# Kernel tuning notes

Measured on AMD Instinct MI355X. Metric: run time of the kernel, lower is better.

Reference implementation:

```python
import jax, jax.numpy as jnp
import numpy as np

N_NODES = 50000
N_EDGES = 800000
IN_DIM = 96
HID = 96
OUT_DIM = 32
N_GRAPHS = 256


def setup_inputs() -> dict:
    key = jax.random.key(0)
    ks = jax.random.split(key, 12)
    x = jax.random.normal(ks[0], (N_NODES, IN_DIM), dtype=jnp.float32)
    edge_index = jax.random.randint(ks[1], (2, N_EDGES), 0, N_NODES, dtype=jnp.int64)
    batch = jnp.sort(jax.random.randint(ks[2], (N_NODES,), 0, N_GRAPHS, dtype=jnp.int64))
    s = 1.0 / np.sqrt(HID)
    W1 = jax.random.normal(ks[3], (IN_DIM, HID), dtype=jnp.float32) * s
    W2 = jax.random.normal(ks[4], (HID, HID), dtype=jnp.float32) * s
    W3 = jax.random.normal(ks[5], (HID, HID), dtype=jnp.float32) * s
    fc_w = jax.random.normal(ks[6], (HID, OUT_DIM), dtype=jnp.float32) * s
    return {
        'x': x, 'edge_index': edge_index, 'batch': batch,
        'W1': W1, 'b1': jnp.zeros((HID,), jnp.float32),
        'W2': W2, 'b2': jnp.zeros((HID,), jnp.float32),
        'W3': W3, 'b3': jnp.zeros((HID,), jnp.float32),
        'fc_w': fc_w, 'fc_b': jnp.zeros((OUT_DIM,), jnp.float32),
    }


def _gcn_conv(h, row, col, norm, W, b, n_nodes):
    # linear transform first (PyG GCNConv), then normalized gather/scatter-add
    h = h @ W                                   # [N, F]
    msg = h[row] * norm[:, None]                # [E+N, F] gather + scale
    out = jax.ops.segment_sum(msg, col, num_segments=n_nodes)
    return out + b


def reference(x, edge_index, batch, W1, b1, W2, b2, W3, b3, fc_w, fc_b):
    n = x.shape[0]
    loop = jnp.arange(n, dtype=edge_index.dtype)
    row = jnp.concatenate([edge_index[0], loop])  # sources (with self-loops)
    col = jnp.concatenate([edge_index[1], loop])  # targets
    # symmetric normalization: deg over targets, norm = d^-1/2[row] * d^-1/2[col]
    deg = jax.ops.segment_sum(jnp.ones_like(col, dtype=x.dtype), col, num_segments=n)
    dis = jnp.where(deg > 0, jax.lax.rsqrt(deg), 0.0)
    norm = dis[row] * dis[col]

    h = jax.nn.relu(_gcn_conv(x, row, col, norm, W1, b1, n))
    h = jax.nn.relu(_gcn_conv(h, row, col, norm, W2, b2, n))
    h = jax.nn.relu(_gcn_conv(h, row, col, norm, W3, b3, n))

    # global_mean_pool over graph ids
    sums = jax.ops.segment_sum(h, batch, num_segments=N_GRAPHS)
    cnts = jax.ops.segment_sum(jnp.ones((n,), h.dtype), batch, num_segments=N_GRAPHS)
    pooled = sums / jnp.maximum(cnts, 1.0)[:, None]
    return pooled @ fc_w + fc_b
```

## Files before the change

kernel.cpp:

```cpp
#include <hip/hip_runtime.h>

#define NN 50000
#define NE 800000
#define F  96
#define F4 24
#define FB 48
#define RB4 12
#define OD 32
#define NG 256
#define CAP 64
#define PROWS 21
#define SHARDS 8
#define SHARD_SZ 6250
#define PERSHARD 64
#define GL 12
#define NWF 1152

typedef unsigned int u32;
typedef unsigned short u16;
typedef short short8 __attribute__((ext_vector_type(8)));
typedef float f32x4 __attribute__((ext_vector_type(4)));

static inline size_t align_up(size_t x) { return (x + 255) & ~(size_t)255; }

__device__ inline u32 f2bf_rne(float x) {
    u32 u = __float_as_uint(x);
    return (u + 0x7fffu + ((u >> 16) & 1u)) >> 16;
}
__device__ inline u32 packbf(float a, float b) {
    return f2bf_rne(a) | (f2bf_rne(b) << 16);
}
__device__ inline float bf_lo(u32 u) { return __uint_as_float(u << 16); }
__device__ inline float bf_hi(u32 u) { return __uint_as_float(u & 0xffff0000u); }

__global__ __launch_bounds__(256) void k_fillb(const int* __restrict__ src,
                                               const int* __restrict__ tgt,
                                               int* __restrict__ cnt,
                                               u16* __restrict__ bucket) {
    int shard = blockIdx.x & (SHARDS - 1);
    int sb    = blockIdx.x >> 3;
    int lo    = shard * SHARD_SZ;
    int hi    = lo + SHARD_SZ;
    const int4* tgt4 = reinterpret_cast<const int4*>(tgt);
    const int4* src4 = reinterpret_cast<const int4*>(src);
    const int nchunk = NE / 4;
    for (int c = sb * 256 + threadIdx.x; c < nchunk; c += PERSHARD * 256) {
        int4 t4 = tgt4[c];
        int4 s4 = src4[c];
        if (t4.x >= lo && t4.x < hi) {
            int p = atomicAdd(&cnt[t4.x], 1);
            if (p < CAP) bucket[t4.x * CAP + p] = (u16)s4.x;
        }
        if (t4.y >= lo && t4.y < hi) {
            int p = atomicAdd(&cnt[t4.y], 1);
            if (p < CAP) bucket[t4.y * CAP + p] = (u16)s4.y;
        }
        if (t4.z >= lo && t4.z < hi) {
            int p = atomicAdd(&cnt[t4.z], 1);
            if (p < CAP) bucket[t4.z * CAP + p] = (u16)s4.z;
        }
        if (t4.w >= lo && t4.w < hi) {
            int p = atomicAdd(&cnt[t4.w], 1);
            if (p < CAP) bucket[t4.w * CAP + p] = (u16)s4.w;
        }
    }
}

__global__ __launch_bounds__(256) void k_dis(const int* __restrict__ cnt, float* __restrict__ dis) {
    int i = blockIdx.x * 256 + threadIdx.x;
    if (i < NN) dis[i] = rsqrtf((float)(cnt[i] + 1));
}

__global__ __launch_bounds__(256) void k_cvt(const float4* __restrict__ x4,
                                             uint4* __restrict__ xb4) {
    int i = blockIdx.x * 256 + threadIdx.x;
    if (i >= NN * RB4) return;
    float4 f0 = x4[(size_t)i * 2];
    float4 f1 = x4[(size_t)i * 2 + 1];
    xb4[i] = make_uint4(packbf(f0.x, f0.y), packbf(f0.z, f0.w),
                        packbf(f1.x, f1.y), packbf(f1.z, f1.w));
}

__global__ __launch_bounds__(256) void k_wprep(const float* __restrict__ W,
                                               uint4* __restrict__ wfragG) {
    int e = blockIdx.x * 256 + threadIdx.x;
    if (e >= NWF) return;
    int n  = e & 15;
    int t1 = e >> 4;
    int quad = t1 & 3;
    int t2 = t1 >> 2;
    int kc = t2 % 3;
    int ct = t2 / 3;
    int k  = kc * 32 + quad * 8;
    int col = ct * 16 + n;
    u32 w0 = packbf(W[(k + 0) * F + col], W[(k + 1) * F + col]);
    u32 w1 = packbf(W[(k + 2) * F + col], W[(k + 3) * F + col]);
    u32 w2 = packbf(W[(k + 4) * F + col], W[(k + 5) * F + col]);
    u32 w3 = packbf(W[(k + 6) * F + col], W[(k + 7) * F + col]);
    wfragG[e] = make_uint4(w0, w1, w2, w3);
}

__global__ __launch_bounds__(256) void k_gemm_mfma(const uint4* __restrict__ Ab4,
                                                   const uint4* __restrict__ wfragG,
                                                   const float* __restrict__ dis,
                                                   u16* __restrict__ Cb16) {
    __shared__ uint4 wfrag[NWF];
    __shared__ uint4 atile[64 * 13];
    int tid = threadIdx.x;
    int r0 = blockIdx.x * 64;
    for (int i = tid; i < NWF; i += 256) wfrag[i] = wfragG[i];
    for (int i = tid; i < 64 * RB4; i += 256) {
        int r = i / RB4, j = i - r * RB4;
        int row = r0 + r;
        atile[r * 13 + j] = (row < NN) ? Ab4[(size_t)row * RB4 + j]
                                       : make_uint4(0u, 0u, 0u, 0u);
    }
    __syncthreads();

    int wave = tid >> 6;
    int lane = tid & 63;
    int m    = lane & 15;
    int quad = lane >> 4;
    int arow = wave * 16 + m;

    short8 a0 = *reinterpret_cast<const short8*>(&atile[arow * 13 + 0 * 4 + quad]);
    short8 a1 = *reinterpret_cast<const short8*>(&atile[arow * 13 + 1 * 4 + quad]);
    short8 a2 = *reinterpret_cast<const short8*>(&atile[arow * 13 + 2 * 4 + quad]);

    f32x4 acc[6];
#pragma unroll
    for (int ct = 0; ct < 6; ++ct) acc[ct] = (f32x4)(0.0f);

#pragma unroll
    for (int ct = 0; ct < 6; ++ct) {
        short8 b0 = *reinterpret_cast<const short8*>(&wfrag[((ct * 3 + 0) * 4 + quad) * 16 + m]);
        short8 b1 = *reinterpret_cast<const short8*>(&wfrag[((ct * 3 + 1) * 4 + quad) * 16 + m]);
        short8 b2 = *reinterpret_cast<const short8*>(&wfrag[((ct * 3 + 2) * 4 + quad) * 16 + m]);
        acc[ct] = __builtin_amdgcn_mfma_f32_16x16x32_bf16(a0, b0, acc[ct], 0, 0, 0);
        acc[ct] = __builtin_amdgcn_mfma_f32_16x16x32_bf16(a1, b1, acc[ct], 0, 0, 0);
        acc[ct] = __builtin_amdgcn_mfma_f32_16x16x32_bf16(a2, b2, acc[ct], 0, 0, 0);
    }

    int rbase = r0 + wave * 16 + quad * 4;
    float dr[4];
#pragma unroll
    for (int r = 0; r < 4; ++r) dr[r] = (rbase + r < NN) ? dis[rbase + r] : 0.0f;
#pragma unroll
    for (int ct = 0; ct < 6; ++ct) {
#pragma unroll
        for (int r = 0; r < 4; ++r) {
            int row = rbase + r;
            if (row < NN)
                Cb16[(size_t)row * F + ct * 16 + m] = (u16)f2bf_rne(acc[ct][r] * dr[r]);
        }
    }
}

__global__ __launch_bounds__(256) void k_gather(const u32* __restrict__ hb,
                                                const int* __restrict__ cnt,
                                                const u16* __restrict__ bucket,
                                                const float* __restrict__ dis,
                                                const float* __restrict__ bias,
                                                uint4* __restrict__ outb4) {
    int idx = blockIdx.x * 256 + threadIdx.x;
    if (idx >= NN * GL) return;
    int v   = idx / GL;
    int sub = idx - v * GL;
    int co  = sub * 4;

    uint4 hv = *reinterpret_cast<const uint4*>(&hb[(size_t)v * FB + co]);
    float a0 = bf_lo(hv.x), a1 = bf_hi(hv.x);
    float a2 = bf_lo(hv.y), a3 = bf_hi(hv.y);
    float a4 = bf_lo(hv.z), a5 = bf_hi(hv.z);
    float a6 = bf_lo(hv.w), a7 = bf_hi(hv.w);

    int deg = cnt[v];
    if (deg > CAP) deg = CAP;
    const u16* bkt = &bucket[v * CAP];

    int e = 0;
    for (; e + 7 < deg; e += 8) {
        uint4 b8 = *reinterpret_cast<const uint4*>(&bkt[e]);
        int s0 = b8.x & 0xffff, s1 = b8.x >> 16;
        int s2 = b8.y & 0xffff, s3 = b8.y >> 16;
        int s4 = b8.z & 0xffff, s5 = b8.z >> 16;
        int s6 = b8.w & 0xffff, s7 = b8.w >> 16;
        uint4 g0 = *reinterpret_cast<const uint4*>(&hb[(size_t)s0 * FB + co]);
        uint4 g1 = *reinterpret_cast<const uint4*>(&hb[(size_t)s1 * FB + co]);
        uint4 g2 = *reinterpret_cast<const uint4*>(&hb[(size_t)s2 * FB + co]);
        uint4 g3 = *reinterpret_cast<const uint4*>(&hb[(size_t)s3 * FB + co]);
        uint4 g4 = *reinterpret_cast<const uint4*>(&hb[(size_t)s4 * FB + co]);
        uint4 g5 = *reinterpret_cast<const uint4*>(&hb[(size_t)s5 * FB + co]);
        uint4 g6 = *reinterpret_cast<const uint4*>(&hb[(size_t)s6 * FB + co]);
        uint4 g7 = *reinterpret_cast<const uint4*>(&hb[(size_t)s7 * FB + co]);
        a0 += bf_lo(g0.x) + bf_lo(g1.x) + bf_lo(g2.x) + bf_lo(g3.x)
            + bf_lo(g4.x) + bf_lo(g5.x) + bf_lo(g6.x) + bf_lo(g7.x);
        a1 += bf_hi(g0.x) + bf_hi(g1.x) + bf_hi(g2.x) + bf_hi(g3.x)
            + bf_hi(g4.x) + bf_hi(g5.x) + bf_hi(g6.x) + bf_hi(g7.x);
        a2 += bf_lo(g0.y) + bf_lo(g1.y) + bf_lo(g2.y) + bf_lo(g3.y)
            + bf_lo(g4.y) + bf_lo(g5.y) + bf_lo(g6.y) + bf_lo(g7.y);
        a3 += bf_hi(g0.y) + bf_hi(g1.y) + bf_hi(g2.y) + bf_hi(g3.y)
            + bf_hi(g4.y) + bf_hi(g5.y) + bf_hi(g6.y) + bf_hi(g7.y);
        a4 += bf_lo(g0.z) + bf_lo(g1.z) + bf_lo(g2.z) + bf_lo(g3.z)
            + bf_lo(g4.z) + bf_lo(g5.z) + bf_lo(g6.z) + bf_lo(g7.z);
        a5 += bf_hi(g0.z) + bf_hi(g1.z) + bf_hi(g2.z) + bf_hi(g3.z)
            + bf_hi(g4.z) + bf_hi(g5.z) + bf_hi(g6.z) + bf_hi(g7.z);
        a6 += bf_lo(g0.w) + bf_lo(g1.w) + bf_lo(g2.w) + bf_lo(g3.w)
            + bf_lo(g4.w) + bf_lo(g5.w) + bf_lo(g6.w) + bf_lo(g7.w);
        a7 += bf_hi(g0.w) + bf_hi(g1.w) + bf_hi(g2.w) + bf_hi(g3.w)
            + bf_hi(g4.w) + bf_hi(g5.w) + bf_hi(g6.w) + bf_hi(g7.w);
    }
    for (; e + 3 < deg; e += 4) {
        uint2 b4 = *reinterpret_cast<const uint2*>(&bkt[e]);
        int s0 = b4.x & 0xffff, s1 = b4.x >> 16;
        int s2 = b4.y & 0xffff, s3 = b4.y >> 16;
        uint4 g0 = *reinterpret_cast<const uint4*>(&hb[(size_t)s0 * FB + co]);
        uint4 g1 = *reinterpret_cast<const uint4*>(&hb[(size_t)s1 * FB + co]);
        uint4 g2 = *reinterpret_cast<const uint4*>(&hb[(size_t)s2 * FB + co]);
        uint4 g3 = *reinterpret_cast<const uint4*>(&hb[(size_t)s3 * FB + co]);
        a0 += bf_lo(g0.x) + bf_lo(g1.x) + bf_lo(g2.x) + bf_lo(g3.x);
        a1 += bf_hi(g0.x) + bf_hi(g1.x) + bf_hi(g2.x) + bf_hi(g3.x);
        a2 += bf_lo(g0.y) + bf_lo(g1.y) + bf_lo(g2.y) + bf_lo(g3.y);
        a3 += bf_hi(g0.y) + bf_hi(g1.y) + bf_hi(g2.y) + bf_hi(g3.y);
        a4 += bf_lo(g0.z) + bf_lo(g1.z) + bf_lo(g2.z) + bf_lo(g3.z);
        a5 += bf_hi(g0.z) + bf_hi(g1.z) + bf_hi(g2.z) + bf_hi(g3.z);
        a6 += bf_lo(g0.w) + bf_lo(g1.w) + bf_lo(g2.w) + bf_lo(g3.w);
        a7 += bf_hi(g0.w) + bf_hi(g1.w) + bf_hi(g2.w) + bf_hi(g3.w);
    }
    for (; e < deg; ++e) {
        int s = bkt[e];
        uint4 g = *reinterpret_cast<const uint4*>(&hb[(size_t)s * FB + co]);
        a0 += bf_lo(g.x); a1 += bf_hi(g.x);
        a2 += bf_lo(g.y); a3 += bf_hi(g.y);
        a4 += bf_lo(g.z); a5 += bf_hi(g.z);
        a6 += bf_lo(g.w); a7 += bf_hi(g.w);
    }
    float dv = dis[v];
    const float4* bb = reinterpret_cast<const float4*>(bias);
    float4 b0 = bb[sub * 2], b1 = bb[sub * 2 + 1];
    float o0 = fmaxf(dv * a0 + b0.x, 0.0f);
    float o1 = fmaxf(dv * a1 + b0.y, 0.0f);
    float o2 = fmaxf(dv * a2 + b0.z, 0.0f);
    float o3 = fmaxf(dv * a3 + b0.w, 0.0f);
    float o4 = fmaxf(dv * a4 + b1.x, 0.0f);
    float o5 = fmaxf(dv * a5 + b1.y, 0.0f);
    float o6 = fmaxf(dv * a6 + b1.z, 0.0f);
    float o7 = fmaxf(dv * a7 + b1.w, 0.0f);
    outb4[(size_t)v * RB4 + sub] = make_uint4(packbf(o0, o1), packbf(o2, o3),
                                              packbf(o4, o5), packbf(o6, o7));
}

__device__ inline int lower_bound_i(const int* __restrict__ a, int n, int key) {
    int lo = 0, hi = n;
    while (lo < hi) {
        int mid = (lo + hi) >> 1;
        if (a[mid] < key) lo = mid + 1; else hi = mid;
    }
    return lo;
}

__global__ __launch_bounds__(512) void k_pool(const uint2* __restrict__ hb2,
                                              const int* __restrict__ batch,
                                              float4* __restrict__ pooled4) {
    __shared__ int range[2];
    __shared__ float4 part[PROWS][F4];
    int g = blockIdx.x;
    int t = threadIdx.x;
    if (t == 0) range[0] = lower_bound_i(batch, NN, g);
    if (t == 1) range[1] = lower_bound_i(batch, NN, g + 1);
    __syncthreads();
    int lo = range[0], hi = range[1];
    int row = t / F4;
    int sub = t - row * F4;
    if (row < PROWS) {
        float4 acc = make_float4(0.f, 0.f, 0.f, 0.f);
        for (int v = lo + row; v < hi; v += PROWS) {
            uint2 xv = hb2[(size_t)v * F4 + sub];
            acc.x += bf_lo(xv.x); acc.y += bf_hi(xv.x);
            acc.z += bf_lo(xv.y); acc.w += bf_hi(xv.y);
        }
        part[row][sub] = acc;
    }
    __syncthreads();
    if (t < F4) {
        float4 s = part[0][t];
        for (int r = 1; r < PROWS; ++r) {
            float4 p = part[r][t];
            s.x += p.x; s.y += p.y; s.z += p.z; s.w += p.w;
        }
        float inv = 1.0f / fmaxf((float)(hi - lo), 1.0f);
        s.x *= inv; s.y *= inv; s.z *= inv; s.w *= inv;
        pooled4[g * F4 + t] = s;
    }
}

__global__ __launch_bounds__(256) void k_fc(const float* __restrict__ pooled,
                                            const float* __restrict__ fcw,
                                            const float* __restrict__ fcb,
                                            float* __restrict__ out) {
    int i = blockIdx.x * 256 + threadIdx.x;
    if (i >= NG * OD) return;
    int g = i >> 5;
    int o = i & 31;
    float acc = 0.0f;
    for (int f = 0; f < F; ++f) acc += pooled[g * F + f] * fcw[f * OD + o];
    out[i] = acc + fcb[o];
}

extern "C" void kernel_launch(void* const* d_in, const int* in_sizes, int n_in,
                              void* d_out, int out_size, void* d_ws, size_t ws_size,
                              hipStream_t stream) {
    (void)in_sizes; (void)n_in; (void)out_size; (void)ws_size;
    const float* x    = (const float*)d_in[0];
    const int*   ei   = (const int*)d_in[1];
    const int*   batc = (const int*)d_in[2];
    const float* W1   = (const float*)d_in[3];
    const float* b1   = (const float*)d_in[4];
    const float* W2   = (const float*)d_in[5];
    const float* b2   = (const float*)d_in[6];
    const float* W3   = (const float*)d_in[7];
    const float* b3   = (const float*)d_in[8];
    const float* fcw  = (const float*)d_in[9];
    const float* fcb  = (const float*)d_in[10];
    float* out = (float*)d_out;

    const int* src = ei;
    const int* tgt = ei + NE;

    char* ws = (char*)d_ws;
    int*    cnt    = (int*)ws;    ws += align_up((size_t)NN * 4);
    float*  dis    = (float*)ws;  ws += align_up((size_t)NN * 4);
    u16*    bucket = (u16*)ws;    ws += align_up((size_t)NN * CAP * 2);
    u32*    hlinb  = (u32*)ws;    ws += align_up((size_t)NN * FB * 4);
    u32*    xb     = (u32*)ws;    ws += align_up((size_t)NN * FB * 4);
    uint4*  wfragG = (uint4*)ws;  ws += align_up((size_t)NWF * 16);
    float*  pooled = (float*)ws;  ws += align_up((size_t)NG * F * 4);

    const int B = 256;
    const int node_grid = (NN + B - 1) / B;
    const int gemm_grid = (NN + 63) / 64;
    const int gath_grid = (NN * GL + B - 1) / B;
    const int cvt_grid  = (NN * RB4 + B - 1) / B;
    const int wprep_grid = (NWF + B - 1) / B;

    (void)hipMemsetAsync(cnt, 0, (size_t)NN * 4, stream);
    k_fillb<<<SHARDS * PERSHARD, B, 0, stream>>>(src, tgt, cnt, bucket);
    k_dis  <<<node_grid, B, 0, stream>>>(cnt, dis);
    k_cvt  <<<cvt_grid, B, 0, stream>>>((const float4*)x, (uint4*)xb);

    k_wprep<<<wprep_grid, B, 0, stream>>>(W1, wfragG);
    k_gemm_mfma<<<gemm_grid, B, 0, stream>>>((const uint4*)xb, wfragG, dis, (u16*)hlinb);
    k_gather<<<gath_grid, B, 0, stream>>>(hlinb, cnt, bucket, dis, b1, (uint4*)xb);

    k_wprep<<<wprep_grid, B, 0, stream>>>(W2, wfragG);
    k_gemm_mfma<<<gemm_grid, B, 0, stream>>>((const uint4*)xb, wfragG, dis, (u16*)hlinb);
    k_gather<<<gath_grid, B, 0, stream>>>(hlinb, cnt, bucket, dis, b2, (uint4*)xb);

    k_wprep<<<wprep_grid, B, 0, stream>>>(W3, wfragG);
    k_gemm_mfma<<<gemm_grid, B, 0, stream>>>((const uint4*)xb, wfragG, dis, (u16*)hlinb);
    k_gather<<<gath_grid, B, 0, stream>>>(hlinb, cnt, bucket, dis, b3, (uint4*)xb);

    k_pool<<<NG, 512, 0, stream>>>((const uint2*)xb, batc, (float4*)pooled);
    k_fc  <<<(NG * OD + B - 1) / B, B, 0, stream>>>(pooled, fcw, fcb, out);
}
```

Baseline: 263.8 us.

## Fuse aggregation and GEMM per layer using aggregate-then-transform ordering

Reorders each GCN layer to aggregate the dis-prescaled features first and then multiply by W, so one kernel does the gather into shared memory followed by the MFMA GEMM with bias, ReLU and next-layer dis scaling in the epilogue. The separate gemm and gather kernels and the intermediate hlin buffer round trip are removed, and the three weight preps are merged into one launch. The cost is a per-block 18KB weight fragment load into LDS for only 32 rows, and the gather's latency is no longer overlapped across separate launches. Rounding also changes slightly because features are stored in bf16 after pre-scaling.

```diff
diff --git a/kernel.cpp b/kernel.cpp
--- a/kernel.cpp
+++ b/kernel.cpp
@@ -13,8 +13,9 @@
 #define SHARDS 8
 #define SHARD_SZ 6250
 #define PERSHARD 64
-#define GL 12
 #define NWF 1152
+#define RPB 32
+#define TPB 128
 
 typedef unsigned int u32;
 typedef unsigned short u16;
@@ -72,21 +73,29 @@
 }
 
 __global__ __launch_bounds__(256) void k_cvt(const float4* __restrict__ x4,
-                                             uint4* __restrict__ xb4) {
+                                             const float* __restrict__ dis,
+                                             uint4* __restrict__ rb4) {
     int i = blockIdx.x * 256 + threadIdx.x;
     if (i >= NN * RB4) return;
+    int v = i / RB4;
+    float dv = dis[v];
     float4 f0 = x4[(size_t)i * 2];
     float4 f1 = x4[(size_t)i * 2 + 1];
-    xb4[i] = make_uint4(packbf(f0.x, f0.y), packbf(f0.z, f0.w),
-                        packbf(f1.x, f1.y), packbf(f1.z, f1.w));
-}
-
-__global__ __launch_bounds__(256) void k_wprep(const float* __restrict__ W,
-                                               uint4* __restrict__ wfragG) {
+    rb4[i] = make_uint4(packbf(dv * f0.x, dv * f0.y), packbf(dv * f0.z, dv * f0.w),
+                        packbf(dv * f1.x, dv * f1.y), packbf(dv * f1.z, dv * f1.w));
+}
+
+__global__ __launch_bounds__(256) void k_wprep3(const float* __restrict__ W1,
+                                                const float* __restrict__ W2,
+                                                const float* __restrict__ W3,
+                                                uint4* __restrict__ wf) {
     int e = blockIdx.x * 256 + threadIdx.x;
-    if (e >= NWF) return;
-    int n  = e & 15;
-    int t1 = e >> 4;
+    if (e >= 3 * NWF) return;
+    int wi = e / NWF;
+    int f  = e - wi * NWF;
+    const float* W = (wi == 0) ? W1 : ((wi == 1) ? W2 : W3);
+    int n  = f & 15;
+    int t1 = f >> 4;
     int quad = t1 & 3;
     int t2 = t1 >> 2;
     int kc = t2 % 3;
@@ -97,23 +106,105 @@
     u32 w1 = packbf(W[(k + 2) * F + col], W[(k + 3) * F + col]);
     u32 w2 = packbf(W[(k + 4) * F + col], W[(k + 5) * F + col]);
     u32 w3 = packbf(W[(k + 6) * F + col], W[(k + 7) * F + col]);
-    wfragG[e] = make_uint4(w0, w1, w2, w3);
-}
-
-__global__ __launch_bounds__(256) void k_gemm_mfma(const uint4* __restrict__ Ab4,
-                                                   const uint4* __restrict__ wfragG,
-                                                   const float* __restrict__ dis,
-                                                   u16* __restrict__ Cb16) {
+    wf[e] = make_uint4(w0, w1, w2, w3);
+}
+
+__global__ __launch_bounds__(TPB) void k_layer(const uint4* __restrict__ rprev,
+                                               const uint4* __restrict__ wfragG,
+                                               const int* __restrict__ cnt,
+                                               const u16* __restrict__ bucket,
+                                               const float* __restrict__ dis,
+                                               const float* __restrict__ bias,
+                                               const int last,
+                                               u16* __restrict__ rnext) {
     __shared__ uint4 wfrag[NWF];
-    __shared__ uint4 atile[64 * 13];
+    __shared__ uint4 atile[RPB * 13];
     int tid = threadIdx.x;
-    int r0 = blockIdx.x * 64;
-    for (int i = tid; i < NWF; i += 256) wfrag[i] = wfragG[i];
-    for (int i = tid; i < 64 * RB4; i += 256) {
-        int r = i / RB4, j = i - r * RB4;
-        int row = r0 + r;
-        atile[r * 13 + j] = (row < NN) ? Ab4[(size_t)row * RB4 + j]
-                                       : make_uint4(0u, 0u, 0u, 0u);
+    int r0 = blockIdx.x * RPB;
+    for (int i = tid; i < NWF; i += TPB) wfrag[i] = wfragG[i];
+
+    const u32* hb = reinterpret_cast<const u32*>(rprev);
+
+#pragma unroll
+    for (int it = 0; it < 3; ++it) {
+        int slot = it * TPB + tid;
+        int ln  = slot / 12;
+        int sub = slot - ln * 12;
+        int v = r0 + ln;
+        uint4 res = make_uint4(0u, 0u, 0u, 0u);
+        if (v < NN) {
+            int co = sub * 4;
+            uint4 hv = *reinterpret_cast<const uint4*>(&hb[(size_t)v * FB + co]);
+            float a0 = bf_lo(hv.x), a1 = bf_hi(hv.x);
+            float a2 = bf_lo(hv.y), a3 = bf_hi(hv.y);
+            float a4 = bf_lo(hv.z), a5 = bf_hi(hv.z);
+            float a6 = bf_lo(hv.w), a7 = bf_hi(hv.w);
+
+            int deg = cnt[v];
+            if (deg > CAP) deg = CAP;
+            const u16* bkt = &bucket[v * CAP];
+            int e = 0;
+            for (; e + 7 < deg; e += 8) {
+                uint4 b8 = *reinterpret_cast<const uint4*>(&bkt[e]);
+                int s0 = b8.x & 0xffff, s1 = b8.x >> 16;
+                int s2 = b8.y & 0xffff, s3 = b8.y >> 16;
+                int s4 = b8.z & 0xffff, s5 = b8.z >> 16;
+                int s6 = b8.w & 0xffff, s7 = b8.w >> 16;
+                uint4 g0 = *reinterpret_cast<const uint4*>(&hb[(size_t)s0 * FB + co]);
+                uint4 g1 = *reinterpret_cast<const uint4*>(&hb[(size_t)s1 * FB + co]);
+                uint4 g2 = *reinterpret_cast<const uint4*>(&hb[(size_t)s2 * FB + co]);
+                uint4 g3 = *reinterpret_cast<const uint4*>(&hb[(size_t)s3 * FB + co]);
+                uint4 g4 = *reinterpret_cast<const uint4*>(&hb[(size_t)s4 * FB + co]);
+                uint4 g5 = *reinterpret_cast<const uint4*>(&hb[(size_t)s5 * FB + co]);
+                uint4 g6 = *reinterpret_cast<const uint4*>(&hb[(size_t)s6 * FB + co]);
+                uint4 g7 = *reinterpret_cast<const uint4*>(&hb[(size_t)s7 * FB + co]);
+                a0 += bf_lo(g0.x) + bf_lo(g1.x) + bf_lo(g2.x) + bf_lo(g3.x)
+                    + bf_lo(g4.x) + bf_lo(g5.x) + bf_lo(g6.x) + bf_lo(g7.x);
+                a1 += bf_hi(g0.x) + bf_hi(g1.x) + bf_hi(g2.x) + bf_hi(g3.x)
+                    + bf_hi(g4.x) + bf_hi(g5.x) + bf_hi(g6.x) + bf_hi(g7.x);
+                a2 += bf_lo(g0.y) + bf_lo(g1.y) + bf_lo(g2.y) + bf_lo(g3.y)
+                    + bf_lo(g4.y) + bf_lo(g5.y) + bf_lo(g6.y) + bf_lo(g7.y);
+                a3 += bf_hi(g0.y) + bf_hi(g1.y) + bf_hi(g2.y) + bf_hi(g3.y)
+                    + bf_hi(g4.y) + bf_hi(g5.y) + bf_hi(g6.y) + bf_hi(g7.y);
+                a4 += bf_lo(g0.z) + bf_lo(g1.z) + bf_lo(g2.z) + bf_lo(g3.z)
+                    + bf_lo(g4.z) + bf_lo(g5.z) + bf_lo(g6.z) + bf_lo(g7.z);
+                a5 += bf_hi(g0.z) + bf_hi(g1.z) + bf_hi(g2.z) + bf_hi(g3.z)
+                    + bf_hi(g4.z) + bf_hi(g5.z) + bf_hi(g6.z) + bf_hi(g7.z);
+                a6 += bf_lo(g0.w) + bf_lo(g1.w) + bf_lo(g2.w) + bf_lo(g3.w)
+                    + bf_lo(g4.w) + bf_lo(g5.w) + bf_lo(g6.w) + bf_lo(g7.w);
+                a7 += bf_hi(g0.w) + bf_hi(g1.w) + bf_hi(g2.w) + bf_hi(g3.w)
+                    + bf_hi(g4.w) + bf_hi(g5.w) + bf_hi(g6.w) + bf_hi(g7.w);
+            }
+            for (; e + 3 < deg; e += 4) {
+                uint2 b4 = *reinterpret_cast<const uint2*>(&bkt[e]);
+                int s0 = b4.x & 0xffff, s1 = b4.x >> 16;
+                int s2 = b4.y & 0xffff, s3 = b4.y >> 16;
+                uint4 g0 = *reinterpret_cast<const uint4*>(&hb[(size_t)s0 * FB + co]);
+                uint4 g1 = *reinterpret_cast<const uint4*>(&hb[(size_t)s1 * FB + co]);
+                uint4 g2 = *reinterpret_cast<const uint4*>(&hb[(size_t)s2 * FB + co]);
+                uint4 g3 = *reinterpret_cast<const uint4*>(&hb[(size_t)s3 * FB + co]);
+                a0 += bf_lo(g0.x) + bf_lo(g1.x) + bf_lo(g2.x) + bf_lo(g3.x);
+                a1 += bf_hi(g0.x) + bf_hi(g1.x) + bf_hi(g2.x) + bf_hi(g3.x);
+                a2 += bf_lo(g0.y) + bf_lo(g1.y) + bf_lo(g2.y) + bf_lo(g3.y);
+                a3 += bf_hi(g0.y) + bf_hi(g1.y) + bf_hi(g2.y) + bf_hi(g3.y);
+                a4 += bf_lo(g0.z) + bf_lo(g1.z) + bf_lo(g2.z) + bf_lo(g3.z);
+                a5 += bf_hi(g0.z) + bf_hi(g1.z) + bf_hi(g2.z) + bf_hi(g3.z);
+                a6 += bf_lo(g0.w) + bf_lo(g1.w) + bf_lo(g2.w) + bf_lo(g3.w);
+                a7 += bf_hi(g0.w) + bf_hi(g1.w) + bf_hi(g2.w) + bf_hi(g3.w);
+            }
+            for (; e < deg; ++e) {
+                int s = bkt[e];
+                uint4 g = *reinterpret_cast<const uint4*>(&hb[(size_t)s * FB + co]);
+                a0 += bf_lo(g.x); a1 += bf_hi(g.x);
+                a2 += bf_lo(g.y); a3 += bf_hi(g.y);
+                a4 += bf_lo(g.z); a5 += bf_hi(g.z);
+                a6 += bf_lo(g.w); a7 += bf_hi(g.w);
+            }
+            float dv = dis[v];
+            res = make_uint4(packbf(dv * a0, dv * a1), packbf(dv * a2, dv * a3),
+                             packbf(dv * a4, dv * a5), packbf(dv * a6, dv * a7));
+        }
+        atile[ln * 13 + sub] = res;
     }
     __syncthreads();
 
@@ -130,7 +221,6 @@
     f32x4 acc[6];
 #pragma unroll
     for (int ct = 0; ct < 6; ++ct) acc[ct] = (f32x4)(0.0f);
-
 #pragma unroll
     for (int ct = 0; ct < 6; ++ct) {
         short8 b0 = *reinterpret_cast<const short8*>(&wfrag[((ct * 3 + 0) * 4 + quad) * 16 + m]);
@@ -144,110 +234,22 @@
     int rbase = r0 + wave * 16 + quad * 4;
     float dr[4];
 #pragma unroll
-    for (int r = 0; r < 4; ++r) dr[r] = (rbase + r < NN) ? dis[rbase + r] : 0.0f;
+    for (int r = 0; r < 4; ++r) {
+        int row = rbase + r;
+        dr[r] = (row < NN) ? (last ? 1.0f : dis[row]) : 0.0f;
+    }
 #pragma unroll
     for (int ct = 0; ct < 6; ++ct) {
+        float bb = bias[ct * 16 + m];
 #pragma unroll
         for (int r = 0; r < 4; ++r) {
             int row = rbase + r;
-            if (row < NN)
-                Cb16[(size_t)row * F + ct * 16 + m] = (u16)f2bf_rne(acc[ct][r] * dr[r]);
-        }
-    }
-}
-
-__global__ __launch_bounds__(256) void k_gather(const u32* __restrict__ hb,
-                                                const int* __restrict__ cnt,
-                                                const u16* __restrict__ bucket,
-                                                const float* __restrict__ dis,
-                                                const float* __restrict__ bias,
-                                                uint4* __restrict__ outb4) {
-    int idx = blockIdx.x * 256 + threadIdx.x;
-    if (idx >= NN * GL) return;
-    int v   = idx / GL;
-    int sub = idx - v * GL;
-    int co  = sub * 4;
-
-    uint4 hv = *reinterpret_cast<const uint4*>(&hb[(size_t)v * FB + co]);
-    float a0 = bf_lo(hv.x), a1 = bf_hi(hv.x);
-    float a2 = bf_lo(hv.y), a3 = bf_hi(hv.y);
-    float a4 = bf_lo(hv.z), a5 = bf_hi(hv.z);
-    float a6 = bf_lo(hv.w), a7 = bf_hi(hv.w);
-
-    int deg = cnt[v];
-    if (deg > CAP) deg = CAP;
-    const u16* bkt = &bucket[v * CAP];
-
-    int e = 0;
-    for (; e + 7 < deg; e += 8) {
-        uint4 b8 = *reinterpret_cast<const uint4*>(&bkt[e]);
-        int s0 = b8.x & 0xffff, s1 = b8.x >> 16;
-        int s2 = b8.y & 0xffff, s3 = b8.y >> 16;
-        int s4 = b8.z & 0xffff, s5 = b8.z >> 16;
-        int s6 = b8.w & 0xffff, s7 = b8.w >> 16;
-        uint4 g0 = *reinterpret_cast<const uint4*>(&hb[(size_t)s0 * FB + co]);
-        uint4 g1 = *reinterpret_cast<const uint4*>(&hb[(size_t)s1 * FB + co]);
-        uint4 g2 = *reinterpret_cast<const uint4*>(&hb[(size_t)s2 * FB + co]);
-        uint4 g3 = *reinterpret_cast<const uint4*>(&hb[(size_t)s3 * FB + co]);
-        uint4 g4 = *reinterpret_cast<const uint4*>(&hb[(size_t)s4 * FB + co]);
-        uint4 g5 = *reinterpret_cast<const uint4*>(&hb[(size_t)s5 * FB + co]);
-        uint4 g6 = *reinterpret_cast<const uint4*>(&hb[(size_t)s6 * FB + co]);
-        uint4 g7 = *reinterpret_cast<const uint4*>(&hb[(size_t)s7 * FB + co]);
-        a0 += bf_lo(g0.x) + bf_lo(g1.x) + bf_lo(g2.x) + bf_lo(g3.x)
-            + bf_lo(g4.x) + bf_lo(g5.x) + bf_lo(g6.x) + bf_lo(g7.x);
-        a1 += bf_hi(g0.x) + bf_hi(g1.x) + bf_hi(g2.x) + bf_hi(g3.x)
-            + bf_hi(g4.x) + bf_hi(g5.x) + bf_hi(g6.x) + bf_hi(g7.x);
-        a2 += bf_lo(g0.y) + bf_lo(g1.y) + bf_lo(g2.y) + bf_lo(g3.y)
-            + bf_lo(g4.y) + bf_lo(g5.y) + bf_lo(g6.y) + bf_lo(g7.y);
-        a3 += bf_hi(g0.y) + bf_hi(g1.y) + bf_hi(g2.y) + bf_hi(g3.y)
-            + bf_hi(g4.y) + bf_hi(g5.y) + bf_hi(g6.y) + bf_hi(g7.y);
-        a4 += bf_lo(g0.z) + bf_lo(g1.z) + bf_lo(g2.z) + bf_lo(g3.z)
-            + bf_lo(g4.z) + bf_lo(g5.z) + bf_lo(g6.z) + bf_lo(g7.z);
-        a5 += bf_hi(g0.z) + bf_hi(g1.z) + bf_hi(g2.z) + bf_hi(g3.z)
-            + bf_hi(g4.z) + bf_hi(g5.z) + bf_hi(g6.z) + bf_hi(g7.z);
-        a6 += bf_lo(g0.w) + bf_lo(g1.w) + bf_lo(g2.w) + bf_lo(g3.w)
-            + bf_lo(g4.w) + bf_lo(g5.w) + bf_lo(g6.w) + bf_lo(g7.w);
-        a7 += bf_hi(g0.w) + bf_hi(g1.w) + bf_hi(g2.w) + bf_hi(g3.w)
-            + bf_hi(g4.w) + bf_hi(g5.w) + bf_hi(g6.w) + bf_hi(g7.w);
-    }
-    for (; e + 3 < deg; e += 4) {
-        uint2 b4 = *reinterpret_cast<const uint2*>(&bkt[e]);
-        int s0 = b4.x & 0xffff, s1 = b4.x >> 16;
-        int s2 = b4.y & 0xffff, s3 = b4.y >> 16;
-        uint4 g0 = *reinterpret_cast<const uint4*>(&hb[(size_t)s0 * FB + co]);
-        uint4 g1 = *reinterpret_cast<const uint4*>(&hb[(size_t)s1 * FB + co]);
-        uint4 g2 = *reinterpret_cast<const uint4*>(&hb[(size_t)s2 * FB + co]);
-        uint4 g3 = *reinterpret_cast<const uint4*>(&hb[(size_t)s3 * FB + co]);
-        a0 += bf_lo(g0.x) + bf_lo(g1.x) + bf_lo(g2.x) + bf_lo(g3.x);
-        a1 += bf_hi(g0.x) + bf_hi(g1.x) + bf_hi(g2.x) + bf_hi(g3.x);
-        a2 += bf_lo(g0.y) + bf_lo(g1.y) + bf_lo(g2.y) + bf_lo(g3.y);
-        a3 += bf_hi(g0.y) + bf_hi(g1.y) + bf_hi(g2.y) + bf_hi(g3.y);
-        a4 += bf_lo(g0.z) + bf_lo(g1.z) + bf_lo(g2.z) + bf_lo(g3.z);
-        a5 += bf_hi(g0.z) + bf_hi(g1.z) + bf_hi(g2.z) + bf_hi(g3.z);
-        a6 += bf_lo(g0.w) + bf_lo(g1.w) + bf_lo(g2.w) + bf_lo(g3.w);
-        a7 += bf_hi(g0.w) + bf_hi(g1.w) + bf_hi(g2.w) + bf_hi(g3.w);
-    }
-    for (; e < deg; ++e) {
-        int s = bkt[e];
-        uint4 g = *reinterpret_cast<const uint4*>(&hb[(size_t)s * FB + co]);
-        a0 += bf_lo(g.x); a1 += bf_hi(g.x);
-        a2 += bf_lo(g.y); a3 += bf_hi(g.y);
-        a4 += bf_lo(g.z); a5 += bf_hi(g.z);
-        a6 += bf_lo(g.w); a7 += bf_hi(g.w);
-    }
-    float dv = dis[v];
-    const float4* bb = reinterpret_cast<const float4*>(bias);
-    float4 b0 = bb[sub * 2], b1 = bb[sub * 2 + 1];
-    float o0 = fmaxf(dv * a0 + b0.x, 0.0f);
-    float o1 = fmaxf(dv * a1 + b0.y, 0.0f);
-    float o2 = fmaxf(dv * a2 + b0.z, 0.0f);
-    float o3 = fmaxf(dv * a3 + b0.w, 0.0f);
-    float o4 = fmaxf(dv * a4 + b1.x, 0.0f);
-    float o5 = fmaxf(dv * a5 + b1.y, 0.0f);
-    float o6 = fmaxf(dv * a6 + b1.z, 0.0f);
-    float o7 = fmaxf(dv * a7 + b1.w, 0.0f);
-    outb4[(size_t)v * RB4 + sub] = make_uint4(packbf(o0, o1), packbf(o2, o3),
-                                              packbf(o4, o5), packbf(o6, o7));
+            if (row < NN) {
+                float h = fmaxf(acc[ct][r] + bb, 0.0f);
+                rnext[(size_t)row * F + ct * 16 + m] = (u16)f2bf_rne(h * dr[r]);
+            }
+        }
+    }
 }
 
 __device__ inline int lower_bound_i(const int* __restrict__ a, int n, int key) {
@@ -331,35 +333,30 @@
     int*    cnt    = (int*)ws;    ws += align_up((size_t)NN * 4);
     float*  dis    = (float*)ws;  ws += align_up((size_t)NN * 4);
     u16*    bucket = (u16*)ws;    ws += align_up((size_t)NN * CAP * 2);
-    u32*    hlinb  = (u32*)ws;    ws += align_up((size_t)NN * FB * 4);
-    u32*    xb     = (u32*)ws;    ws += align_up((size_t)NN * FB * 4);
-    uint4*  wfragG = (uint4*)ws;  ws += align_up((size_t)NWF * 16);
+    u32*    rA     = (u32*)ws;    ws += align_up((size_t)NN * FB * 4);
+    u32*    rB     = (u32*)ws;    ws += align_up((size_t)NN * FB * 4);
+    uint4*  wfrag3 = (uint4*)ws;  ws += align_up((size_t)3 * NWF * 16);
     float*  pooled = (float*)ws;  ws += align_up((size_t)NG * F * 4);
 
     const int B = 256;
-    const int node_grid = (NN + B - 1) / B;
-    const int gemm_grid = (NN + 63) / 64;
-    const int gath_grid = (NN * GL + B - 1) / B;
-    const int cvt_grid  = (NN * RB4 + B - 1) / B;
-    const int wprep_grid = (NWF + B - 1) / B;
+    const int node_grid  = (NN + B - 1) / B;
+    const int cvt_grid   = (NN * RB4 + B - 1) / B;
+    const int wprep_grid = (3 * NWF + B - 1) / B;
+    const int layer_grid = (NN + RPB - 1) / RPB;
 
     (void)hipMemsetAsync(cnt, 0, (size_t)NN * 4, stream);
-    k_fillb<<<SHARDS * PERSHARD, B, 0, stream>>>(src, tgt, cnt, bucket);
-    k_dis  <<<node_grid, B, 0, stream>>>(cnt, dis);
-    k_cvt  <<<cvt_grid, B, 0, stream>>>((const float4*)x, (uint4*)xb);
-
-    k_wprep<<<wprep_grid, B, 0, stream>>>(W1, wfragG);
-    k_gemm_mfma<<<gemm_grid, B, 0, stream>>>((const uint4*)xb, wfragG, dis, (u16*)hlinb);
-    k_gather<<<gath_grid, B, 0, stream>>>(hlinb, cnt, bucket, dis, b1, (uint4*)xb);
-
-    k_wprep<<<wprep_grid, B, 0, stream>>>(W2, wfragG);
-    k_gemm_mfma<<<gemm_grid, B, 0, stream>>>((const uint4*)xb, wfragG, dis, (u16*)hlinb);
-    k_gather<<<gath_grid, B, 0, stream>>>(hlinb, cnt, bucket, dis, b2, (uint4*)xb);
-
-    k_wprep<<<wprep_grid, B, 0, stream>>>(W3, wfragG);
-    k_gemm_mfma<<<gemm_grid, B, 0, stream>>>((const uint4*)xb, wfragG, dis, (u16*)hlinb);
-    k_gather<<<gath_grid, B, 0, stream>>>(hlinb, cnt, bucket, dis, b3, (uint4*)xb);
-
-    k_pool<<<NG, 512, 0, stream>>>((const uint2*)xb, batc, (float4*)pooled);
+    k_fillb <<<SHARDS * PERSHARD, B, 0, stream>>>(src, tgt, cnt, bucket);
+    k_dis   <<<node_grid, B, 0, stream>>>(cnt, dis);
+    k_wprep3<<<wprep_grid, B, 0, stream>>>(W1, W2, W3, wfrag3);
+    k_cvt   <<<cvt_grid, B, 0, stream>>>((const float4*)x, dis, (uint4*)rA);
+
+    k_layer<<<layer_grid, TPB, 0, stream>>>((const uint4*)rA, wfrag3 + 0 * NWF,
+                                            cnt, bucket, dis, b1, 0, (u16*)rB);
+    k_layer<<<layer_grid, TPB, 0, stream>>>((const uint4*)rB, wfrag3 + 1 * NWF,
+                                            cnt, bucket, dis, b2, 0, (u16*)rA);
+    k_layer<<<layer_grid, TPB, 0, stream>>>((const uint4*)rA, wfrag3 + 2 * NWF,
+                                            cnt, bucket, dis, b3, 1, (u16*)rB);
+
+    k_pool<<<NG, 512, 0, stream>>>((const uint2*)rB, batc, (float4*)pooled);
     k_fc  <<<(NG * OD + B - 1) / B, B, 0, stream>>>(pooled, fcw, fcb, out);
 }
```

Result: slower. 290.0 us (+9.9%).
